# Performance work log

Measured on AMD Instinct MI355X. Metric: run time of the kernel, lower is better.

Reference implementation:

```python
import jax, jax.numpy as jnp
import numpy as np

DIM = 768
HEADS = 12
HEAD_DIM = DIM // HEADS
ROPE_BASE = 100.0  # Dust3R uses freq=100 for its rotary embedding


def apply_rope(x):
    # x: [B, H, N, D] -> rotary embedding over token index (rotate-half form)
    B, H, N, D = x.shape
    pos = jnp.arange(N, dtype=jnp.float32)
    inv_freq = 1.0 / (ROPE_BASE ** (jnp.arange(0, D, 2, dtype=jnp.float32) / D))
    ang = pos[:, None] * inv_freq[None, :]            # [N, D/2]
    cos = jnp.concatenate([jnp.cos(ang), jnp.cos(ang)], axis=-1).astype(x.dtype)  # [N, D]
    sin = jnp.concatenate([jnp.sin(ang), jnp.sin(ang)], axis=-1).astype(x.dtype)
    x1, x2 = jnp.split(x, 2, axis=-1)
    x_rot = jnp.concatenate([-x2, x1], axis=-1)
    return x * cos + x_rot * sin


def setup_inputs() -> dict:
    key = jax.random.key(0)
    ks = jax.random.split(key, 8)
    B, N = 8, 1024
    scale = 0.02
    return {
        "query": jax.random.normal(ks[0], (B, N, DIM), jnp.float32),
        "key": jax.random.normal(ks[1], (B, N, DIM), jnp.float32),
        "value": jax.random.normal(ks[2], (B, N, DIM), jnp.float32),
        "Wq": jax.random.normal(ks[3], (DIM, DIM), jnp.float32) * scale,
        "Wk": jax.random.normal(ks[4], (DIM, DIM), jnp.float32) * scale,
        "Wv": jax.random.normal(ks[5], (DIM, DIM), jnp.float32) * scale,
        "Wo": jax.random.normal(ks[6], (DIM, DIM), jnp.float32) * scale,
        "bo": jax.random.normal(ks[7], (DIM,), jnp.float32) * scale,
    }


def reference(query, key, value, Wq, Wk, Wv, Wo, bo):
    B, Nq, C = query.shape
    H, D = HEADS, HEAD_DIM
    sm_scale = D ** -0.5
    # Linear projections (torch Linear: x @ W.T), split heads -> [B, H, N, D]
    q = jnp.einsum('bnc,dc->bnd', query, Wq).reshape(B, Nq, H, D).transpose(0, 2, 1, 3)
    k = jnp.einsum('bnc,dc->bnd', key, Wk).reshape(B, -1, H, D).transpose(0, 2, 1, 3)
    v = jnp.einsum('bnc,dc->bnd', value, Wv).reshape(B, -1, H, D).transpose(0, 2, 1, 3)
    q = apply_rope(q)
    k = apply_rope(k)
    attn = jnp.einsum('bhqd,bhkd->bhqk', q, k) * sm_scale
    attn = jax.nn.softmax(attn, axis=-1)
    x = jnp.einsum('bhqk,bhkd->bhqd', attn, v)
    x = x.transpose(0, 2, 1, 3).reshape(B, Nq, C)
    return jnp.einsum('bnc,dc->bnd', x, Wo) + bo
```

## Files before the change

### kernel.cpp

```cpp
#include <hip/hip_runtime.h>
#include <cmath>

typedef __bf16 bf16x8 __attribute__((ext_vector_type(8)));
typedef float f32x4 __attribute__((ext_vector_type(4)));
typedef unsigned short u16;

#define MFMA_BF16 __builtin_amdgcn_mfma_f32_16x16x32_bf16

__device__ __forceinline__ u16 f2bf(float f) {
  unsigned int u = __float_as_uint(f);
  u = (u + 0x7fffu + ((u >> 16) & 1u)) >> 16;
  return (u16)u;
}

__device__ __forceinline__ void async16(const u16* g, u16* l) {
  __builtin_amdgcn_global_load_lds(
      (__attribute__((address_space(1))) void*)g,
      (__attribute__((address_space(3))) void*)l, 16, 0, 0);
}

__global__ __launch_bounds__(256) void cvt_bf16(const float4* __restrict__ in,
                                                uint2* __restrict__ out, int n4) {
  int i = blockIdx.x * 256 + threadIdx.x;
  if (i >= n4) return;
  float4 f = in[i];
  uint2 o;
  o.x = (unsigned)f2bf(f.x) | ((unsigned)f2bf(f.y) << 16);
  o.y = (unsigned)f2bf(f.z) | ((unsigned)f2bf(f.w) << 16);
  out[i] = o;
}

__global__ __launch_bounds__(256) void cvt_all(
    const float4* s0, const float4* s1, const float4* s2, const float4* s3,
    const float4* s4, const float4* s5, const float4* s6,
    uint2* d0, uint2* d1, uint2* d2, uint2* d3, uint2* d4, uint2* d5, uint2* d6) {
  int i = blockIdx.x * 256 + threadIdx.x;
  const float4* src;
  uint2* dst;
  int off;
  if (i < 1572864)      { src = s0; dst = d0; off = i; }
  else if (i < 3145728) { src = s1; dst = d1; off = i - 1572864; }
  else if (i < 4718592) { src = s2; dst = d2; off = i - 3145728; }
  else {
    int j = i - 4718592;
    int w = j / 147456;
    off = j - w * 147456;
    src = (w == 0) ? s3 : (w == 1) ? s4 : (w == 2) ? s5 : s6;
    dst = (w == 0) ? d3 : (w == 1) ? d4 : (w == 2) ? d5 : d6;
  }
  float4 f = src[off];
  uint2 o;
  o.x = (unsigned)f2bf(f.x) | ((unsigned)f2bf(f.y) << 16);
  o.y = (unsigned)f2bf(f.z) | ((unsigned)f2bf(f.w) << 16);
  dst[off] = o;
}

__device__ __forceinline__ void gemm_body(const u16* __restrict__ Ag,
                                          const u16* __restrict__ Wg,
                                          void* __restrict__ OutP,
                                          const float* __restrict__ bias,
                                          int mode, int bx, int by) {
  __shared__ u16 As[128][64];
  __shared__ u16 Bs[64][64];
  const int tid  = threadIdx.x;
  const int lane = tid & 63, wv = tid >> 6;
  const int l15  = lane & 15, quad = lane >> 4;
  const int row0 = bx * 128, col0 = by * 64;
  const int wm = wv * 32;
  const int swA = l15 & 7;

  f32x4 acc[2][4];
#pragma unroll
  for (int i = 0; i < 2; ++i)
#pragma unroll
    for (int j = 0; j < 4; ++j) acc[i][j] = (f32x4){0.f, 0.f, 0.f, 0.f};

  for (int kb0 = 0; kb0 < 768; kb0 += 64) {
#pragma unroll
    for (int rr = 0; rr < 4; ++rr) {
      int c = rr * 256 + tid;
      int row = c >> 3, cp = c & 7;
      int gc = cp ^ (row & 7);
      async16(&Ag[(size_t)(row0 + row) * 768 + kb0 + gc * 8], &As[row][cp * 8]);
    }
#pragma unroll
    for (int rr = 0; rr < 2; ++rr) {
      int c = rr * 256 + tid;
      int row = c >> 3, cp = c & 7;
      int gc = cp ^ (row & 7);
      async16(&Wg[(size_t)(col0 + row) * 768 + kb0 + gc * 8], &Bs[row][cp * 8]);
    }
    __syncthreads();
#pragma unroll
    for (int kd = 0; kd < 2; ++kd) {
      int cpk = (((kd * 4 + quad) ^ swA)) * 8;
      bf16x8 af[2], bfr[4];
      af[0] = *(const bf16x8*)&As[wm + l15][cpk];
      af[1] = *(const bf16x8*)&As[wm + 16 + l15][cpk];
#pragma unroll
      for (int nt = 0; nt < 4; ++nt) bfr[nt] = *(const bf16x8*)&Bs[nt * 16 + l15][cpk];
#pragma unroll
      for (int mt = 0; mt < 2; ++mt)
#pragma unroll
        for (int nt = 0; nt < 4; ++nt)
          acc[mt][nt] = MFMA_BF16(af[mt], bfr[nt], acc[mt][nt], 0, 0, 0);
    }
    __syncthreads();
  }

  if (mode == 3) {
    float* O = (float*)OutP;
#pragma unroll
    for (int mt = 0; mt < 2; ++mt)
#pragma unroll
      for (int r = 0; r < 4; ++r) {
        int m = row0 + wm + mt * 16 + quad * 4 + r;
#pragma unroll
        for (int nt = 0; nt < 4; ++nt) {
          int c = col0 + nt * 16 + l15;
          O[(size_t)m * 768 + c] = acc[mt][nt][r] + bias[c];
        }
      }
  } else if (mode == 2) {
    u16* O = (u16*)OutP;
#pragma unroll
    for (int mt = 0; mt < 2; ++mt)
#pragma unroll
      for (int r = 0; r < 4; ++r) {
        int m = row0 + wm + mt * 16 + quad * 4 + r;
        int b = m >> 10, n = m & 1023;
#pragma unroll
        for (int nt = 0; nt < 4; ++nt) {
          int c = col0 + nt * 16 + l15;
          O[(size_t)(b * 768 + c) * 1024 + n] = f2bf(acc[mt][nt][r]);
        }
      }
  } else {
    u16* O = (u16*)OutP;
    const float scale = (mode == 0) ? 0.125f * 1.44269504088896f : 1.0f;
    const float invf0 = exp2f(-6.6438561897747395f * (float)l15 * (1.0f / 32.0f));
    const float invf1 = exp2f(-6.6438561897747395f * (float)(16 + l15) * (1.0f / 32.0f));
#pragma unroll
    for (int mt = 0; mt < 2; ++mt)
#pragma unroll
      for (int r = 0; r < 4; ++r) {
        int m = row0 + wm + mt * 16 + quad * 4 + r;
        int b = m >> 10, n = m & 1023;
        float fn = (float)n;
        size_t rowbase = (size_t)b * 786432 + (size_t)n * 64;
#pragma unroll
        for (int nt = 0; nt < 2; ++nt) {
          float sv, cv;
          __sincosf(fn * (nt ? invf1 : invf0), &sv, &cv);
          float x1 = acc[mt][nt][r], x2 = acc[mt][nt + 2][r];
          int c1 = col0 + nt * 16 + l15;
          int c2 = c1 + 32;
          O[rowbase + (size_t)(c1 >> 6) * 65536 + (c1 & 63)] = f2bf((x1 * cv - x2 * sv) * scale);
          O[rowbase + (size_t)(c2 >> 6) * 65536 + (c2 & 63)] = f2bf((x2 * cv + x1 * sv) * scale);
        }
      }
  }
}

__global__ __launch_bounds__(256, 3) void gemm768(const u16* __restrict__ A,
                                                  const u16* __restrict__ W,
                                                  void* __restrict__ OutP,
                                                  const float* __restrict__ bias,
                                                  int mode) {
  gemm_body(A, W, OutP, bias, mode, blockIdx.x, blockIdx.y);
}

__global__ __launch_bounds__(256, 3) void gemm_qkv(
    const u16* __restrict__ xq, const u16* __restrict__ xk, const u16* __restrict__ xv,
    const u16* __restrict__ wq, const u16* __restrict__ wk, const u16* __restrict__ wv,
    u16* __restrict__ qb, u16* __restrict__ kb, u16* __restrict__ vtb) {
  int z = blockIdx.z;
  const u16* A = (z == 0) ? xq : (z == 1) ? xk : xv;
  const u16* W = (z == 0) ? wq : (z == 1) ? wk : wv;
  void* O      = (z == 0) ? (void*)qb : (z == 1) ? (void*)kb : (void*)vtb;
  gemm_body(A, W, O, nullptr, z, blockIdx.x, blockIdx.y);
}

__global__ __launch_bounds__(256, 2) void attn_fused(const u16* __restrict__ Q,
                                                     const u16* __restrict__ K,
                                                     const u16* __restrict__ Vt,
                                                     u16* __restrict__ X) {
  __shared__ u16 KsF[2 * 64 * 32];
  __shared__ u16 VsF[2 * 64 * 32];
  __shared__ u16 Ps[128 * 88];

  const int tid  = threadIdx.x;
  const int lane = tid & 63, wv = tid >> 6;
  const int l15  = lane & 15, quad = lane >> 4;
  const int bh = blockIdx.x, qt = blockIdx.y;
  const size_t base = (size_t)bh * 65536;
  const int sw8 = (quad ^ ((l15 >> 1) & 3)) * 8;

  const u16* Qg = Q + base + (size_t)qt * 8192;
#pragma unroll
  for (int rr = 0; rr < 4; ++rr) {
    int c = rr * 256 + tid;
    async16(&Qg[c * 8], &Ps[c * 8]);
  }
  __syncthreads();
  bf16x8 qf[2][2];
#pragma unroll
  for (int mt = 0; mt < 2; ++mt)
#pragma unroll
    for (int kd = 0; kd < 2; ++kd)
      qf[mt][kd] = *(const bf16x8*)&Ps[(wv * 32 + mt * 16 + l15) * 64 + kd * 32 + quad * 8];
  __syncthreads();

  f32x4 o[2][4];
  float lsum[2][4];
#pragma unroll
  for (int mt = 0; mt < 2; ++mt) {
#pragma unroll
    for (int nt = 0; nt < 4; ++nt) o[mt][nt] = (f32x4){0.f, 0.f, 0.f, 0.f};
#pragma unroll
    for (int r = 0; r < 4; ++r) lsum[mt][r] = 0.f;
  }

  const u16* Kb = K + base;
  const u16* Vb = Vt + base;

  for (int kt = 0; kt < 1024; kt += 64) {
#pragma unroll
    for (int rr = 0; rr < 2; ++rr) {
      int c = rr * 256 + tid;
      int sub = c >> 8, rowi = (c >> 2) & 63, colc = c & 3;
      int cs = (colc ^ ((rowi >> 1) & 3)) * 8;
      async16(&Kb[(size_t)(kt + rowi) * 64 + sub * 32 + cs], &KsF[c * 8]);
      async16(&Vb[(size_t)rowi * 1024 + kt + sub * 32 + cs], &VsF[c * 8]);
    }
    __syncthreads();

    f32x4 s[2][4];
#pragma unroll
    for (int ct = 0; ct < 4; ++ct) {
      bf16x8 kf0 = *(const bf16x8*)&KsF[(ct * 16 + l15) * 32 + sw8];
      bf16x8 kf1 = *(const bf16x8*)&KsF[2048 + (ct * 16 + l15) * 32 + sw8];
#pragma unroll
      for (int mt = 0; mt < 2; ++mt) {
        f32x4 t = (f32x4){0.f, 0.f, 0.f, 0.f};
        t = MFMA_BF16(qf[mt][0], kf0, t, 0, 0, 0);
        t = MFMA_BF16(qf[mt][1], kf1, t, 0, 0, 0);
        s[mt][ct] = t;
      }
    }

#pragma unroll
    for (int mt = 0; mt < 2; ++mt)
#pragma unroll
      for (int ct = 0; ct < 4; ++ct)
#pragma unroll
        for (int r = 0; r < 4; ++r) {
          float p = __builtin_amdgcn_exp2f(s[mt][ct][r]);
          lsum[mt][r] += p;
          unsigned u = __float_as_uint(p);
          Ps[(wv * 32 + mt * 16 + quad * 4 + r) * 88 + ct * 16 + l15] =
              (u16)((u + 0x8000u) >> 16);
        }

#pragma unroll
    for (int ks = 0; ks < 2; ++ks) {
      bf16x8 pf0 = *(const bf16x8*)&Ps[(wv * 32 + l15) * 88 + ks * 32 + quad * 8];
      bf16x8 pf1 = *(const bf16x8*)&Ps[(wv * 32 + 16 + l15) * 88 + ks * 32 + quad * 8];
#pragma unroll
      for (int nt = 0; nt < 4; ++nt) {
        bf16x8 vf = *(const bf16x8*)&VsF[ks * 2048 + (nt * 16 + l15) * 32 + sw8];
        o[0][nt] = MFMA_BF16(pf0, vf, o[0][nt], 0, 0, 0);
        o[1][nt] = MFMA_BF16(pf1, vf, o[1][nt], 0, 0, 0);
      }
    }
    __syncthreads();
  }

  const int b = bh / 12, h = bh % 12;
#pragma unroll
  for (int mt = 0; mt < 2; ++mt)
#pragma unroll
    for (int r = 0; r < 4; ++r) {
      float l = lsum[mt][r];
#pragma unroll
      for (int d = 1; d < 16; d <<= 1) l += __shfl_xor(l, d, 16);
      float inv = __builtin_amdgcn_rcpf(l);
      int n = qt * 128 + wv * 32 + mt * 16 + quad * 4 + r;
      size_t rowoff = ((size_t)(b * 1024 + n)) * 768 + h * 64;
#pragma unroll
      for (int nt = 0; nt < 4; ++nt)
        X[rowoff + nt * 16 + l15] = f2bf(o[mt][nt][r] * inv);
    }
}

extern "C" void kernel_launch(void* const* d_in, const int* in_sizes, int n_in,
                              void* d_out, int out_size, void* d_ws, size_t ws_size,
                              hipStream_t stream) {
  const float* qin = (const float*)d_in[0];
  const float* kin = (const float*)d_in[1];
  const float* vin = (const float*)d_in[2];
  const float* Wq  = (const float*)d_in[3];
  const float* Wk  = (const float*)d_in[4];
  const float* Wv  = (const float*)d_in[5];
  const float* Wo  = (const float*)d_in[6];
  const float* bo  = (const float*)d_in[7];
  char* ws = (char*)d_ws;

  if (ws_size >= 80216064) {
    u16* xq16 = (u16*)(ws + 0);
    u16* xk16 = (u16*)(ws + 12582912);
    u16* xv16 = (u16*)(ws + 25165824);
    u16* qb   = (u16*)(ws + 37748736);
    u16* kb   = (u16*)(ws + 50331648);
    u16* vtb  = (u16*)(ws + 62914560);
    u16* wq16 = (u16*)(ws + 75497472);
    u16* wk16 = wq16 + 589824;
    u16* wv16 = wk16 + 589824;
    u16* wo16 = wv16 + 589824;
    u16* X    = xq16;

    cvt_all<<<20736, 256, 0, stream>>>(
        (const float4*)qin, (const float4*)kin, (const float4*)vin,
        (const float4*)Wq, (const float4*)Wk, (const float4*)Wv, (const float4*)Wo,
        (uint2*)xq16, (uint2*)xk16, (uint2*)xv16,
        (uint2*)wq16, (uint2*)wk16, (uint2*)wv16, (uint2*)wo16);
    gemm_qkv<<<dim3(64, 12, 3), 256, 0, stream>>>(xq16, xk16, xv16, wq16, wk16, wv16,
                                                  qb, kb, vtb);
    attn_fused<<<dim3(96, 8), 256, 0, stream>>>(qb, kb, vtb, X);
    gemm768<<<dim3(64, 12), 256, 0, stream>>>(X, wo16, d_out, bo, 3);
  } else {
    u16* xbuf = (u16*)(ws + 0);
    u16* qb   = (u16*)(ws + 12582912);
    u16* kb   = (u16*)(ws + 25165824);
    u16* vtb  = (u16*)(ws + 37748736);
    u16* wq16 = (u16*)(ws + 50331648);
    u16* wk16 = wq16 + 589824;
    u16* wv16 = wk16 + 589824;
    u16* wo16 = wv16 + 589824;

    cvt_bf16<<<576, 256, 0, stream>>>((const float4*)Wq, (uint2*)wq16, 147456);
    cvt_bf16<<<576, 256, 0, stream>>>((const float4*)Wk, (uint2*)wk16, 147456);
    cvt_bf16<<<576, 256, 0, stream>>>((const float4*)Wv, (uint2*)wv16, 147456);
    cvt_bf16<<<576, 256, 0, stream>>>((const float4*)Wo, (uint2*)wo16, 147456);

    dim3 ggrid(64, 12);
    cvt_bf16<<<6144, 256, 0, stream>>>((const float4*)qin, (uint2*)xbuf, 1572864);
    gemm768<<<ggrid, 256, 0, stream>>>(xbuf, wq16, (void*)qb, nullptr, 0);
    cvt_bf16<<<6144, 256, 0, stream>>>((const float4*)kin, (uint2*)xbuf, 1572864);
    gemm768<<<ggrid, 256, 0, stream>>>(xbuf, wk16, (void*)kb, nullptr, 1);
    cvt_bf16<<<6144, 256, 0, stream>>>((const float4*)vin, (uint2*)xbuf, 1572864);
    gemm768<<<ggrid, 256, 0, stream>>>(xbuf, wv16, (void*)vtb, nullptr, 2);

    attn_fused<<<dim3(96, 8), 256, 0, stream>>>(qb, kb, vtb, xbuf);

    gemm768<<<ggrid, 256, 0, stream>>>(xbuf, wo16, d_out, bo, 3);
  }
}
```

Measured before the change: 224.0 us.

## Double-buffer GEMM and attention LDS tiles and transpose attention MFMA operands

Both the projection GEMM and the attention kernel now double-buffer their LDS tiles, issuing the async global-to-LDS loads for the next k-tile before computing the current one. This is meant to hide global load latency behind MFMA work. The attention kernel also swaps the MFMA operand order so each lane holds one query row's scores. That allows vectorized 8-byte P stores into per-wave LDS slices, a simpler row-sum reduction and vectorized output stores. Occupancy hint is raised to 3 blocks, and LDS use grows, which risks register or LDS pressure limiting occupancy.

Result: faster. 219.2 us (-2.2%).

```diff
diff --git a/kernel.cpp b/kernel.cpp
--- a/kernel.cpp
+++ b/kernel.cpp
@@ -11,6 +11,10 @@
   unsigned int u = __float_as_uint(f);
   u = (u + 0x7fffu + ((u >> 16) & 1u)) >> 16;
   return (u16)u;
+}
+
+__device__ __forceinline__ unsigned pbf(float f) {
+  return (__float_as_uint(f) + 0x8000u) >> 16;
 }
 
 __device__ __forceinline__ void async16(const u16* g, u16* l) {
@@ -60,8 +64,8 @@
                                           void* __restrict__ OutP,
                                           const float* __restrict__ bias,
                                           int mode, int bx, int by) {
-  __shared__ u16 As[128][64];
-  __shared__ u16 Bs[64][64];
+  __shared__ alignas(16) u16 As[2][128][64];
+  __shared__ alignas(16) u16 Bs[2][64][64];
   const int tid  = threadIdx.x;
   const int lane = tid & 63, wv = tid >> 6;
   const int l15  = lane & 15, quad = lane >> 4;
@@ -69,36 +73,51 @@
   const int wm = wv * 32;
   const int swA = l15 & 7;
 
+  size_t aSrc[4], bSrc[2];
+  int aDst[4], bDst[2];
+#pragma unroll
+  for (int rr = 0; rr < 4; ++rr) {
+    int c = rr * 256 + tid;
+    int row = c >> 3, cp = c & 7;
+    int gc = cp ^ (row & 7);
+    aSrc[rr] = (size_t)(row0 + row) * 768 + gc * 8;
+    aDst[rr] = c * 8;
+  }
+#pragma unroll
+  for (int rr = 0; rr < 2; ++rr) {
+    int c = rr * 256 + tid;
+    int row = c >> 3, cp = c & 7;
+    int gc = cp ^ (row & 7);
+    bSrc[rr] = (size_t)(col0 + row) * 768 + gc * 8;
+    bDst[rr] = c * 8;
+  }
+
+  auto stage = [&](int kb, int bf) {
+#pragma unroll
+    for (int rr = 0; rr < 4; ++rr) async16(&Ag[aSrc[rr] + kb], &((u16*)As[bf])[aDst[rr]]);
+#pragma unroll
+    for (int rr = 0; rr < 2; ++rr) async16(&Wg[bSrc[rr] + kb], &((u16*)Bs[bf])[bDst[rr]]);
+  };
+
   f32x4 acc[2][4];
 #pragma unroll
   for (int i = 0; i < 2; ++i)
 #pragma unroll
     for (int j = 0; j < 4; ++j) acc[i][j] = (f32x4){0.f, 0.f, 0.f, 0.f};
 
-  for (int kb0 = 0; kb0 < 768; kb0 += 64) {
-#pragma unroll
-    for (int rr = 0; rr < 4; ++rr) {
-      int c = rr * 256 + tid;
-      int row = c >> 3, cp = c & 7;
-      int gc = cp ^ (row & 7);
-      async16(&Ag[(size_t)(row0 + row) * 768 + kb0 + gc * 8], &As[row][cp * 8]);
-    }
-#pragma unroll
-    for (int rr = 0; rr < 2; ++rr) {
-      int c = rr * 256 + tid;
-      int row = c >> 3, cp = c & 7;
-      int gc = cp ^ (row & 7);
-      async16(&Wg[(size_t)(col0 + row) * 768 + kb0 + gc * 8], &Bs[row][cp * 8]);
-    }
-    __syncthreads();
+  stage(0, 0);
+  __syncthreads();
+
+  auto step = [&](int kb, int rb) {
+    if (kb < 704) stage(kb + 64, rb ^ 1);
 #pragma unroll
     for (int kd = 0; kd < 2; ++kd) {
       int cpk = (((kd * 4 + quad) ^ swA)) * 8;
       bf16x8 af[2], bfr[4];
-      af[0] = *(const bf16x8*)&As[wm + l15][cpk];
-      af[1] = *(const bf16x8*)&As[wm + 16 + l15][cpk];
-#pragma unroll
-      for (int nt = 0; nt < 4; ++nt) bfr[nt] = *(const bf16x8*)&Bs[nt * 16 + l15][cpk];
+      af[0] = *(const bf16x8*)&As[rb][wm + l15][cpk];
+      af[1] = *(const bf16x8*)&As[rb][wm + 16 + l15][cpk];
+#pragma unroll
+      for (int nt = 0; nt < 4; ++nt) bfr[nt] = *(const bf16x8*)&Bs[rb][nt * 16 + l15][cpk];
 #pragma unroll
       for (int mt = 0; mt < 2; ++mt)
 #pragma unroll
@@ -106,6 +125,11 @@
           acc[mt][nt] = MFMA_BF16(af[mt], bfr[nt], acc[mt][nt], 0, 0, 0);
     }
     __syncthreads();
+  };
+
+  for (int kb = 0; kb < 768; kb += 128) {
+    step(kb, 0);
+    step(kb + 64, 1);
   }
 
   if (mode == 3) {
@@ -181,13 +205,13 @@
   gemm_body(A, W, O, nullptr, z, blockIdx.x, blockIdx.y);
 }
 
-__global__ __launch_bounds__(256, 2) void attn_fused(const u16* __restrict__ Q,
+__global__ __launch_bounds__(256, 3) void attn_fused(const u16* __restrict__ Q,
                                                      const u16* __restrict__ K,
                                                      const u16* __restrict__ Vt,
                                                      u16* __restrict__ X) {
-  __shared__ u16 KsF[2 * 64 * 32];
-  __shared__ u16 VsF[2 * 64 * 32];
-  __shared__ u16 Ps[128 * 88];
+  __shared__ alignas(16) u16 KsF[2][4096];
+  __shared__ alignas(16) u16 VsF[2][4096];
+  __shared__ alignas(16) u16 Ps[4][2304];
 
   const int tid  = threadIdx.x;
   const int lane = tid & 63, wv = tid >> 6;
@@ -197,100 +221,124 @@
   const int sw8 = (quad ^ ((l15 >> 1) & 3)) * 8;
 
   const u16* Qg = Q + base + (size_t)qt * 8192;
+  const u16* Kb = K + base;
+  const u16* Vb = Vt + base;
+
+  int kOff[2], vOff[2], dOff[2];
+#pragma unroll
+  for (int rr = 0; rr < 2; ++rr) {
+    int c = rr * 256 + tid;
+    int sub = c >> 8, rowi = (c >> 2) & 63, colc = c & 3;
+    int cs = (colc ^ ((rowi >> 1) & 3)) * 8;
+    kOff[rr] = rowi * 64 + sub * 32 + cs;
+    vOff[rr] = rowi * 1024 + sub * 32 + cs;
+    dOff[rr] = c * 8;
+  }
+
+  auto stageKV = [&](int kt, int bf) {
+#pragma unroll
+    for (int rr = 0; rr < 2; ++rr) {
+      async16(&Kb[(size_t)kt * 64 + kOff[rr]], &KsF[bf][dOff[rr]]);
+      async16(&Vb[(size_t)kt + vOff[rr]], &VsF[bf][dOff[rr]]);
+    }
+  };
+
+  u16* Pflat = &Ps[0][0];
 #pragma unroll
   for (int rr = 0; rr < 4; ++rr) {
     int c = rr * 256 + tid;
-    async16(&Qg[c * 8], &Ps[c * 8]);
-  }
+    async16(&Qg[c * 8], &Pflat[c * 8]);
+  }
+  stageKV(0, 0);
   __syncthreads();
+
   bf16x8 qf[2][2];
 #pragma unroll
   for (int mt = 0; mt < 2; ++mt)
 #pragma unroll
     for (int kd = 0; kd < 2; ++kd)
-      qf[mt][kd] = *(const bf16x8*)&Ps[(wv * 32 + mt * 16 + l15) * 64 + kd * 32 + quad * 8];
+      qf[mt][kd] = *(const bf16x8*)&Pflat[(wv * 32 + mt * 16 + l15) * 64 + kd * 32 + quad * 8];
   __syncthreads();
 
   f32x4 o[2][4];
-  float lsum[2][4];
+  float lsum[2] = {0.f, 0.f};
+#pragma unroll
+  for (int mt = 0; mt < 2; ++mt)
+#pragma unroll
+    for (int nt = 0; nt < 4; ++nt) o[mt][nt] = (f32x4){0.f, 0.f, 0.f, 0.f};
+
+  u16* Pw = &Ps[wv][0];
+  const int prow0 = l15 * 72, prow1 = (16 + l15) * 72;
+
+  auto tile = [&](int t, int rb) {
+    if (t < 15) stageKV((t + 1) * 64, rb ^ 1);
+
+    f32x4 s[2][4];
+#pragma unroll
+    for (int ct = 0; ct < 4; ++ct) {
+      bf16x8 kf0 = *(const bf16x8*)&KsF[rb][(ct * 16 + l15) * 32 + sw8];
+      bf16x8 kf1 = *(const bf16x8*)&KsF[rb][2048 + (ct * 16 + l15) * 32 + sw8];
+#pragma unroll
+      for (int mt = 0; mt < 2; ++mt) {
+        f32x4 tacc = (f32x4){0.f, 0.f, 0.f, 0.f};
+        tacc = MFMA_BF16(kf0, qf[mt][0], tacc, 0, 0, 0);
+        tacc = MFMA_BF16(kf1, qf[mt][1], tacc, 0, 0, 0);
+        s[mt][ct] = tacc;
+      }
+    }
+
+#pragma unroll
+    for (int mt = 0; mt < 2; ++mt) {
+#pragma unroll
+      for (int ct = 0; ct < 4; ++ct) {
+        float p0 = __builtin_amdgcn_exp2f(s[mt][ct][0]);
+        float p1 = __builtin_amdgcn_exp2f(s[mt][ct][1]);
+        float p2 = __builtin_amdgcn_exp2f(s[mt][ct][2]);
+        float p3 = __builtin_amdgcn_exp2f(s[mt][ct][3]);
+        lsum[mt] += (p0 + p1) + (p2 + p3);
+        uint2 w;
+        w.x = pbf(p0) | (pbf(p1) << 16);
+        w.y = pbf(p2) | (pbf(p3) << 16);
+        *(uint2*)&Pw[(mt ? prow1 : prow0) + ct * 16 + quad * 4] = w;
+      }
+    }
+
+#pragma unroll
+    for (int ks = 0; ks < 2; ++ks) {
+      bf16x8 pf0 = *(const bf16x8*)&Pw[prow0 + ks * 32 + quad * 8];
+      bf16x8 pf1 = *(const bf16x8*)&Pw[prow1 + ks * 32 + quad * 8];
+#pragma unroll
+      for (int nt = 0; nt < 4; ++nt) {
+        bf16x8 vf = *(const bf16x8*)&VsF[rb][ks * 2048 + (nt * 16 + l15) * 32 + sw8];
+        o[0][nt] = MFMA_BF16(vf, pf0, o[0][nt], 0, 0, 0);
+        o[1][nt] = MFMA_BF16(vf, pf1, o[1][nt], 0, 0, 0);
+      }
+    }
+    __syncthreads();
+  };
+
+  for (int t = 0; t < 16; t += 2) {
+    tile(t, 0);
+    tile(t + 1, 1);
+  }
+
+  const int b = bh / 12, h = bh % 12;
 #pragma unroll
   for (int mt = 0; mt < 2; ++mt) {
-#pragma unroll
-    for (int nt = 0; nt < 4; ++nt) o[mt][nt] = (f32x4){0.f, 0.f, 0.f, 0.f};
-#pragma unroll
-    for (int r = 0; r < 4; ++r) lsum[mt][r] = 0.f;
-  }
-
-  const u16* Kb = K + base;
-  const u16* Vb = Vt + base;
-
-  for (int kt = 0; kt < 1024; kt += 64) {
-#pragma unroll
-    for (int rr = 0; rr < 2; ++rr) {
-      int c = rr * 256 + tid;
-      int sub = c >> 8, rowi = (c >> 2) & 63, colc = c & 3;
-      int cs = (colc ^ ((rowi >> 1) & 3)) * 8;
-      async16(&Kb[(size_t)(kt + rowi) * 64 + sub * 32 + cs], &KsF[c * 8]);
-      async16(&Vb[(size_t)rowi * 1024 + kt + sub * 32 + cs], &VsF[c * 8]);
-    }
-    __syncthreads();
-
-    f32x4 s[2][4];
-#pragma unroll
-    for (int ct = 0; ct < 4; ++ct) {
-      bf16x8 kf0 = *(const bf16x8*)&KsF[(ct * 16 + l15) * 32 + sw8];
-      bf16x8 kf1 = *(const bf16x8*)&KsF[2048 + (ct * 16 + l15) * 32 + sw8];
-#pragma unroll
-      for (int mt = 0; mt < 2; ++mt) {
-        f32x4 t = (f32x4){0.f, 0.f, 0.f, 0.f};
-        t = MFMA_BF16(qf[mt][0], kf0, t, 0, 0, 0);
-        t = MFMA_BF16(qf[mt][1], kf1, t, 0, 0, 0);
-        s[mt][ct] = t;
-      }
-    }
-
-#pragma unroll
-    for (int mt = 0; mt < 2; ++mt)
-#pragma unroll
-      for (int ct = 0; ct < 4; ++ct)
-#pragma unroll
-        for (int r = 0; r < 4; ++r) {
-          float p = __builtin_amdgcn_exp2f(s[mt][ct][r]);
-          lsum[mt][r] += p;
-          unsigned u = __float_as_uint(p);
-          Ps[(wv * 32 + mt * 16 + quad * 4 + r) * 88 + ct * 16 + l15] =
-              (u16)((u + 0x8000u) >> 16);
-        }
-
-#pragma unroll
-    for (int ks = 0; ks < 2; ++ks) {
-      bf16x8 pf0 = *(const bf16x8*)&Ps[(wv * 32 + l15) * 88 + ks * 32 + quad * 8];
-      bf16x8 pf1 = *(const bf16x8*)&Ps[(wv * 32 + 16 + l15) * 88 + ks * 32 + quad * 8];
-#pragma unroll
-      for (int nt = 0; nt < 4; ++nt) {
-        bf16x8 vf = *(const bf16x8*)&VsF[ks * 2048 + (nt * 16 + l15) * 32 + sw8];
-        o[0][nt] = MFMA_BF16(pf0, vf, o[0][nt], 0, 0, 0);
-        o[1][nt] = MFMA_BF16(pf1, vf, o[1][nt], 0, 0, 0);
-      }
-    }
-    __syncthreads();
-  }
-
-  const int b = bh / 12, h = bh % 12;
-#pragma unroll
-  for (int mt = 0; mt < 2; ++mt)
-#pragma unroll
-    for (int r = 0; r < 4; ++r) {
-      float l = lsum[mt][r];
-#pragma unroll
-      for (int d = 1; d < 16; d <<= 1) l += __shfl_xor(l, d, 16);
-      float inv = __builtin_amdgcn_rcpf(l);
-      int n = qt * 128 + wv * 32 + mt * 16 + quad * 4 + r;
-      size_t rowoff = ((size_t)(b * 1024 + n)) * 768 + h * 64;
-#pragma unroll
-      for (int nt = 0; nt < 4; ++nt)
-        X[rowoff + nt * 16 + l15] = f2bf(o[mt][nt][r] * inv);
-    }
+    float l = lsum[mt];
+    l += __shfl_xor(l, 16);
+    l += __shfl_xor(l, 32);
+    float inv = __builtin_amdgcn_rcpf(l);
+    int n = qt * 128 + wv * 32 + mt * 16 + l15;
+    size_t rowoff = ((size_t)(b * 1024 + n)) * 768 + h * 64 + quad * 4;
+#pragma unroll
+    for (int nt = 0; nt < 4; ++nt) {
+      uint2 w;
+      w.x = (unsigned)f2bf(o[mt][nt][0] * inv) | ((unsigned)f2bf(o[mt][nt][1] * inv) << 16);
+      w.y = (unsigned)f2bf(o[mt][nt][2] * inv) | ((unsigned)f2bf(o[mt][nt][3] * inv) << 16);
+      *(uint2*)&X[rowoff + nt * 16] = w;
+    }
+  }
 }
 
 extern "C" void kernel_launch(void* const* d_in, const int* in_sizes, int n_in,
```
